# Performance work log

Hardware: AMD Instinct MI355X
Metric: run time of the kernel (lower is better)

## Reference

```python
import jax, jax.numpy as jnp
import numpy as np

N = 100000
E = 1600000
D_IN = 64
D_HID = 64
D_OUT = 64


def setup_inputs() -> dict:
    key = jax.random.key(0)
    ks = jax.random.split(key, 12)
    x = jax.random.normal(ks[0], (N, D_IN), dtype=jnp.float32)
    edge_index = jax.random.randint(ks[1], (2, E), 0, N, dtype=jnp.int64)
    s1 = 1.0 / np.sqrt(D_IN)
    s2 = 1.0 / np.sqrt(D_HID)
    return {
        "x": x,
        "edge_index": edge_index,
        "W1l": jax.random.uniform(ks[2], (D_HID, D_IN), jnp.float32, -s1, s1),
        "b1l": jax.random.uniform(ks[3], (D_HID,), jnp.float32, -s1, s1),
        "W1r": jax.random.uniform(ks[4], (D_HID, D_IN), jnp.float32, -s1, s1),
        "W2l": jax.random.uniform(ks[5], (D_HID, D_HID), jnp.float32, -s2, s2),
        "b2l": jax.random.uniform(ks[6], (D_HID,), jnp.float32, -s2, s2),
        "W2r": jax.random.uniform(ks[7], (D_HID, D_HID), jnp.float32, -s2, s2),
        "Wout": jax.random.uniform(ks[8], (D_OUT, D_HID), jnp.float32, -s2, s2),
        "bout": jax.random.uniform(ks[9], (D_OUT,), jnp.float32, -s2, s2),
        "drop": 0,
    }


def _sage_conv(x, src, dst, Wl, bl, Wr, n_nodes):
    # PyG SAGEConv, aggr='mean': out = lin_l(mean_j x_j) + lin_r(x_i)
    msg = x[src]                                            # [E, d] gather
    agg = jax.ops.segment_sum(msg, dst, num_segments=n_nodes)
    deg = jax.ops.segment_sum(jnp.ones((src.shape[0],), x.dtype), dst,
                              num_segments=n_nodes)
    mean = agg / jnp.maximum(deg, 1.0)[:, None]             # empty neighborhoods -> 0
    return mean @ Wl.T + bl + x @ Wr.T


def reference(x, edge_index, W1l, b1l, W1r, W2l, b2l, W2r, Wout, bout, drop):
    src, dst = edge_index[0], edge_index[1]
    n = x.shape[0]
    # dropout is identity in eval mode (training=False); drop unused
    h = jax.nn.relu(_sage_conv(x, src, dst, W1l, b1l, W1r, n))
    h = jax.nn.relu(_sage_conv(h, src, dst, W2l, b2l, W2r, n))
    logits = h @ Wout.T + bout
    return jax.nn.log_softmax(logits, axis=1)
```

## Files before the change

kernel.cpp:

```cpp
#include <hip/hip_runtime.h>


#define TB 256
#define TBA 1024
#define NBINA 256
#define XFB 512
#define CAPC 32
#define NBPAD 1024
#define SP 68

typedef __attribute__((ext_vector_type(8))) short bf16x8;
typedef __attribute__((ext_vector_type(4))) float f32x4;
typedef __attribute__((ext_vector_type(2))) float f32x2;

__device__ __forceinline__ unsigned short bf16c(float f) {
  union { float f; unsigned u; } v; v.f = f;
  unsigned r = (v.u + 0x7FFFu + ((v.u >> 16) & 1u)) >> 16;
  return (unsigned short)r;
}

__device__ __forceinline__ bf16x8 ld_bf8(const float* p) {
  float4 a = *(const float4*)p;
  float4 b = *(const float4*)(p + 4);
  bf16x8 r;
  r[0] = bf16c(a.x); r[1] = bf16c(a.y); r[2] = bf16c(a.z); r[3] = bf16c(a.w);
  r[4] = bf16c(b.x); r[5] = bf16c(b.y); r[6] = bf16c(b.z); r[7] = bf16c(b.w);
  return r;
}

__device__ __forceinline__ float bflo(unsigned u) { return __uint_as_float(u << 16); }
__device__ __forceinline__ float bfhi(unsigned u) { return __uint_as_float(u & 0xFFFF0000u); }
__device__ __forceinline__ unsigned bfpk(float lo, float hi) {
  return (unsigned)bf16c(lo) | ((unsigned)bf16c(hi) << 16);
}

__global__ __launch_bounds__(1024) void k_binA(
    const int* __restrict__ ei, int E,
    int* __restrict__ cellcnt, unsigned int* __restrict__ bucketData, int NB) {
  __shared__ int lcnt[NBPAD];
  __shared__ int s_nz;
  if (threadIdx.x == 0) s_nz = 0;
  for (int i = threadIdx.x; i < NBPAD; i += TBA) lcnt[i] = 0;
  __syncthreads();
  int nz = 0;
  for (int i = threadIdx.x; i < 2048; i += TBA) nz |= ei[2 * i + 1];
  if (nz) atomicOr(&s_nz, 1);
  __syncthreads();
  bool m64 = (s_nz == 0);
  int bb = blockIdx.x;

  long long e0 = (long long)E * bb / NBINA;
  long long e1 = (long long)E * (bb + 1) / NBINA;
  for (long long e = e0 + threadIdx.x; e < e1; e += TBA) {
    int src, dst;
    if (m64) {
      src = ((const int2*)ei)[e].x;
      dst = ((const int2*)ei)[(long long)E + e].x;
    } else {
      src = ei[e];
      dst = ei[(long long)E + e];
    }
    int b = dst >> 7;
    int pos = atomicAdd(&lcnt[b], 1);
    if (pos < CAPC)
      bucketData[((size_t)b * NBINA + bb) * CAPC + pos] =
          ((unsigned)(dst & 127) << 24) | (unsigned)src;
  }
  __syncthreads();
  for (int b = threadIdx.x; b < NB; b += TBA) cellcnt[bb * NBPAD + b] = lcnt[b];
}

__global__ __launch_bounds__(256) void k_binB(
    const unsigned int* __restrict__ bucketData, const int* __restrict__ cellcnt,
    int* __restrict__ colp, int* __restrict__ cnt) {
  __shared__ unsigned int slice[128 * SP];
  __shared__ int lcnt[128];
  int b = blockIdx.x;
  for (int i = threadIdx.x; i < 128; i += TB) lcnt[i] = 0;
  __syncthreads();
  int c = cellcnt[threadIdx.x * NBPAD + b];
  if (c > CAPC) c = CAPC;
  const uint4* cell4 =
      (const uint4*)(bucketData + ((size_t)b * NBINA + threadIdx.x) * CAPC);
#pragma unroll
  for (int k4 = 0; k4 < CAPC / 4; ++k4) {
    if (k4 * 4 >= c) break;
    uint4 r4 = cell4[k4];
#pragma unroll
    for (int j = 0; j < 4; ++j) {
      int k = k4 * 4 + j;
      if (k < c) {
        unsigned rec = (&r4.x)[j];
        int dl = rec >> 24;
        int pos = atomicAdd(&lcnt[dl], 1);
        if (pos < 64) slice[dl * SP + pos] = rec & 0xFFFFFFu;
      }
    }
  }
  __syncthreads();
  size_t obase = (size_t)b * (128 * 64);
  for (int i = threadIdx.x * 4; i < 128 * 64; i += TB * 4) {
    int node = i >> 6, j = i & 63;
    *(uint4*)(colp + obase + i) = *(const uint4*)(slice + node * SP + j);
  }
  int node0 = b << 7;
  for (int i = threadIdx.x; i < 128; i += TB) cnt[node0 + i] = lcnt[i];
}

__global__ __launch_bounds__(256) void k_xform_f32(
    const float* __restrict__ xin, const float* __restrict__ Wl,
    const float* __restrict__ Wr, const float* __restrict__ bl,
    unsigned short* __restrict__ y, unsigned short* __restrict__ zout, int n) {
  int lane = threadIdx.x & 63;
  int quad = lane >> 4, m = lane & 15;
  int w0 = (blockIdx.x * blockDim.x + threadIdx.x) >> 6;
  int nw = (gridDim.x * blockDim.x) >> 6;

  bf16x8 bfrag[8][2];
  float bias[4];
#pragma unroll
  for (int t = 0; t < 8; ++t) {
    const float* W = (t < 4) ? Wl : Wr;
    int row = (t & 3) * 16 + m;
#pragma unroll
    for (int s = 0; s < 2; ++s)
      bfrag[t][s] = ld_bf8(W + row * 64 + s * 32 + quad * 8);
  }
#pragma unroll
  for (int t = 0; t < 4; ++t) bias[t] = bl[t * 16 + m];

  int nT = (n + 15) >> 4;
  for (int tile = w0; tile < nT; tile += nw) {
    int node0 = tile << 4;
    int mrow = node0 + m;
    if (mrow >= n) mrow = n - 1;
    const float* xr = xin + (size_t)mrow * 64;
    bf16x8 a0 = ld_bf8(xr + quad * 8);
    bf16x8 a1 = ld_bf8(xr + 32 + quad * 8);

    f32x4 acc[8];
#pragma unroll
    for (int t = 0; t < 8; ++t) {
      f32x4 z4 = {0.f, 0.f, 0.f, 0.f};
      z4 = __builtin_amdgcn_mfma_f32_16x16x32_bf16(a0, bfrag[t][0], z4, 0, 0, 0);
      acc[t] = __builtin_amdgcn_mfma_f32_16x16x32_bf16(a1, bfrag[t][1], z4, 0, 0, 0);
    }

#pragma unroll
    for (int r = 0; r < 4; ++r) {
      int node = node0 + quad * 4 + r;
      if (node >= n) break;
      size_t rb = (size_t)node * 64 + m;
#pragma unroll
      for (int t = 0; t < 4; ++t) y[rb + t * 16] = bf16c(acc[t][r]);
#pragma unroll
      for (int t = 0; t < 4; ++t) zout[rb + t * 16] = bf16c(acc[t + 4][r] + bias[t]);
    }
  }
}

__global__ __launch_bounds__(256) void k_xform_b16(
    const unsigned short* zin, const float* __restrict__ Wl,
    const float* __restrict__ Wr, const float* __restrict__ bl,
    unsigned short* __restrict__ y, unsigned short* zout, int n) {
  int lane = threadIdx.x & 63;
  int quad = lane >> 4, m = lane & 15;
  int w0 = (blockIdx.x * blockDim.x + threadIdx.x) >> 6;
  int nw = (gridDim.x * blockDim.x) >> 6;

  bf16x8 bfrag[8][2];
  float bias[4];
#pragma unroll
  for (int t = 0; t < 8; ++t) {
    const float* W = (t < 4) ? Wl : Wr;
    int row = (t & 3) * 16 + m;
#pragma unroll
    for (int s = 0; s < 2; ++s)
      bfrag[t][s] = ld_bf8(W + row * 64 + s * 32 + quad * 8);
  }
#pragma unroll
  for (int t = 0; t < 4; ++t) bias[t] = bl[t * 16 + m];

  int nT = (n + 15) >> 4;
  for (int tile = w0; tile < nT; tile += nw) {
    int node0 = tile << 4;
    int mrow = node0 + m;
    if (mrow >= n) mrow = n - 1;
    const unsigned short* xr = zin + (size_t)mrow * 64;
    bf16x8 a0 = *(const bf16x8*)(xr + quad * 8);
    bf16x8 a1 = *(const bf16x8*)(xr + 32 + quad * 8);

    f32x4 acc[8];
#pragma unroll
    for (int t = 0; t < 8; ++t) {
      f32x4 z4 = {0.f, 0.f, 0.f, 0.f};
      z4 = __builtin_amdgcn_mfma_f32_16x16x32_bf16(a0, bfrag[t][0], z4, 0, 0, 0);
      acc[t] = __builtin_amdgcn_mfma_f32_16x16x32_bf16(a1, bfrag[t][1], z4, 0, 0, 0);
    }

#pragma unroll
    for (int r = 0; r < 4; ++r) {
      int node = node0 + quad * 4 + r;
      if (node >= n) break;
      size_t rb = (size_t)node * 64 + m;
#pragma unroll
      for (int t = 0; t < 4; ++t) y[rb + t * 16] = bf16c(acc[t][r]);
#pragma unroll
      for (int t = 0; t < 4; ++t) zout[rb + t * 16] = bf16c(acc[t + 4][r] + bias[t]);
    }
  }
}

__global__ __launch_bounds__(256) void k_aggr(
    const unsigned short* __restrict__ yb, const int* __restrict__ cnt,
    const int* __restrict__ colp, unsigned short* zio, int n) {
  const unsigned int* y = (const unsigned int*)yb;
  int lane = threadIdx.x & 63;
  int wv = (blockIdx.x * blockDim.x + threadIdx.x) >> 6;
  int g16 = lane & 48;
  int lig = lane & 15;
  int sub = lig >> 3;
  int fo = (lig & 7) * 4;

  int node = (wv << 2) + (g16 >> 4);
  bool act = node < n;
  int cn = act ? node : 0;
  int deg = cnt[cn];
  int jcap = deg < 64 ? deg : 64;
  size_t crow = (size_t)cn << 6;
  int cidxA = colp[crow + lig];
  int cidxB = colp[crow + 16 + lig];

  int wmax = jcap;
  wmax = max(wmax, __shfl_xor(wmax, 16, 64));
  wmax = max(wmax, __shfl_xor(wmax, 32, 64));

  f32x2 acc[4];
#pragma unroll
  for (int k = 0; k < 4; ++k) acc[k] = (f32x2){0.f, 0.f};

#define ACCUM(U)                                             \
  do {                                                       \
    acc[0] += (f32x2){bflo((U).x), bfhi((U).x)};             \
    acc[1] += (f32x2){bflo((U).y), bfhi((U).y)};             \
    acc[2] += (f32x2){bflo((U).z), bfhi((U).z)};             \
    acc[3] += (f32x2){bflo((U).w), bfhi((U).w)};             \
  } while (0)

#pragma unroll
  for (int s = 0; s < 32; s += 2) {
    int slot = s + sub;
    int c = (s < 16) ? __shfl(cidxA, g16 | slot, 64)
                     : __shfl(cidxB, g16 | (slot - 16), 64);
    if (slot < jcap) {
      uint4 v = *(const uint4*)(y + ((size_t)c << 5) + fo);
      ACCUM(v);
    }
  }
  if (wmax > 32) {
    int cidxC = colp[crow + 32 + lig];
    int cidxD = colp[crow + 48 + lig];
    {
      int lim = (wmax < 48 ? wmax : 48) - 32;
      for (int s = 0; s < lim; s += 2) {
        int slot = s + sub;
        int c = __shfl(cidxC, g16 | slot, 64);
        if (slot + 32 < jcap) {
          uint4 v = *(const uint4*)(y + ((size_t)c << 5) + fo);
          ACCUM(v);
        }
      }
    }
    if (wmax > 48) {
      int lim = wmax - 48;
      for (int s = 0; s < lim; s += 2) {
        int slot = s + sub;
        int c = __shfl(cidxD, g16 | slot, 64);
        if (slot + 48 < jcap) {
          uint4 v = *(const uint4*)(y + ((size_t)c << 5) + fo);
          ACCUM(v);
        }
      }
    }
  }
#undef ACCUM

#pragma unroll
  for (int k = 0; k < 4; ++k) {
    acc[k].x += __shfl_xor(acc[k].x, 8, 64);
    acc[k].y += __shfl_xor(acc[k].y, 8, 64);
  }

  if (act && sub == 0) {
    float inv = (deg > 0) ? 1.0f / (float)deg : 0.f;
    unsigned int* zp = (unsigned int*)(zio + ((size_t)node << 6)) + fo;
    uint4 zv = *(uint4*)zp;
    zv.x = bfpk(fmaxf(fmaf(acc[0].x, inv, bflo(zv.x)), 0.f),
                fmaxf(fmaf(acc[0].y, inv, bfhi(zv.x)), 0.f));
    zv.y = bfpk(fmaxf(fmaf(acc[1].x, inv, bflo(zv.y)), 0.f),
                fmaxf(fmaf(acc[1].y, inv, bfhi(zv.y)), 0.f));
    zv.z = bfpk(fmaxf(fmaf(acc[2].x, inv, bflo(zv.z)), 0.f),
                fmaxf(fmaf(acc[2].y, inv, bfhi(zv.z)), 0.f));
    zv.w = bfpk(fmaxf(fmaf(acc[3].x, inv, bflo(zv.w)), 0.f),
                fmaxf(fmaf(acc[3].y, inv, bfhi(zv.w)), 0.f));
    *(uint4*)zp = zv;
  }
}

__global__ __launch_bounds__(256) void k_out(
    const unsigned short* __restrict__ h, const float* __restrict__ Wo,
    const float* __restrict__ bo, float* __restrict__ out, int n) {
  int lane = threadIdx.x & 63;
  int quad = lane >> 4, m = lane & 15;
  int w0 = (blockIdx.x * blockDim.x + threadIdx.x) >> 6;
  int nw = (gridDim.x * blockDim.x) >> 6;

  bf16x8 bfrag[4][2];
  float bias[4];
#pragma unroll
  for (int t = 0; t < 4; ++t) {
    int row = t * 16 + m;
#pragma unroll
    for (int s = 0; s < 2; ++s)
      bfrag[t][s] = ld_bf8(Wo + row * 64 + s * 32 + quad * 8);
    bias[t] = bo[t * 16 + m];
  }

  int nT = (n + 15) >> 4;
  for (int tile = w0; tile < nT; tile += nw) {
    int node0 = tile << 4;
    int mrow = node0 + m;
    if (mrow >= n) mrow = n - 1;
    const unsigned short* xr = h + (size_t)mrow * 64;
    bf16x8 a0 = *(const bf16x8*)(xr + quad * 8);
    bf16x8 a1 = *(const bf16x8*)(xr + 32 + quad * 8);

    f32x4 acc[4];
#pragma unroll
    for (int t = 0; t < 4; ++t) {
      f32x4 z4 = {0.f, 0.f, 0.f, 0.f};
      z4 = __builtin_amdgcn_mfma_f32_16x16x32_bf16(a0, bfrag[t][0], z4, 0, 0, 0);
      acc[t] = __builtin_amdgcn_mfma_f32_16x16x32_bf16(a1, bfrag[t][1], z4, 0, 0, 0);
    }

#pragma unroll
    for (int r = 0; r < 4; ++r) {
      int node = node0 + quad * 4 + r;
      if (node >= n) break;
      float l0 = acc[0][r] + bias[0];
      float l1 = acc[1][r] + bias[1];
      float l2 = acc[2][r] + bias[2];
      float l3 = acc[3][r] + bias[3];
      float mx = fmaxf(fmaxf(l0, l1), fmaxf(l2, l3));
#pragma unroll
      for (int off = 1; off <= 8; off <<= 1) mx = fmaxf(mx, __shfl_xor(mx, off, 64));
      float s = expf(l0 - mx) + expf(l1 - mx) + expf(l2 - mx) + expf(l3 - mx);
#pragma unroll
      for (int off = 1; off <= 8; off <<= 1) s += __shfl_xor(s, off, 64);
      float ls = logf(s);
      size_t rb = (size_t)node * 64 + m;
      out[rb + 0]  = l0 - mx - ls;
      out[rb + 16] = l1 - mx - ls;
      out[rb + 32] = l2 - mx - ls;
      out[rb + 48] = l3 - mx - ls;
    }
  }
}

extern "C" void kernel_launch(void* const* d_in, const int* in_sizes, int n_in,
                              void* d_out, int out_size, void* d_ws, size_t ws_size,
                              hipStream_t stream) {
  const float* x    = (const float*)d_in[0];
  const int*   ei   = (const int*)d_in[1];
  const float* W1l  = (const float*)d_in[2];
  const float* b1l  = (const float*)d_in[3];
  const float* W1r  = (const float*)d_in[4];
  const float* W2l  = (const float*)d_in[5];
  const float* b2l  = (const float*)d_in[6];
  const float* W2r  = (const float*)d_in[7];
  const float* Wout = (const float*)d_in[8];
  const float* bout = (const float*)d_in[9];
  int N = in_sizes[0] / 64;
  int E = in_sizes[1] / 2;
  int NB = (N + 127) >> 7;

  char* p = (char*)d_ws;
  auto carve = [&](size_t bytes) {
    char* r = p;
    p += (bytes + 255) & ~(size_t)255;
    return r;
  };
  int* cellcnt       = (int*)carve((size_t)NBINA * NBPAD * 4);
  int* cnt           = (int*)carve((size_t)NB * 128 * 4);
  int* colp          = (int*)carve((size_t)NB * 128 * 64 * 4);
  unsigned short* y  = (unsigned short*)carve((size_t)N * 64 * 2);
  unsigned short* z  = (unsigned short*)carve((size_t)N * 64 * 2);
  unsigned int* bucketData = (unsigned int*)carve((size_t)NB * NBINA * CAPC * 4);

  int aggr_blocks = (N + 15) / 16;
  k_binA<<<NBINA, TBA, 0, stream>>>(ei, E, cellcnt, bucketData, NB);
  k_binB<<<NB, TB, 0, stream>>>(bucketData, cellcnt, colp, cnt);
  k_xform_f32<<<XFB, TB, 0, stream>>>(x, W1l, W1r, b1l, y, z, N);
  k_aggr<<<aggr_blocks, TB, 0, stream>>>(y, cnt, colp, z, N);
  k_xform_b16<<<XFB, TB, 0, stream>>>(z, W2l, W2r, b2l, y, z, N);
  k_aggr<<<aggr_blocks, TB, 0, stream>>>(y, cnt, colp, z, N);
  k_out<<<XFB, TB, 0, stream>>>(z, Wout, bout, (float*)d_out, N);
}
```

Before: 236.9 us.

## Fuse bucket finalization into aggregation kernel, drop materialized CSR arrays

Merges the second binning pass (k_binB) into the aggregation kernel. Each layer's aggregation block now rebuilds its 128-node neighbor slice in shared memory from the bucket data and gathers neighbor features straight from that slice. This removes one launch and the write and read of the padded colp and cnt arrays. In exchange the slice construction is done twice (once per layer), blocks become coarser (128 nodes each, one per wave group over 8 iterations), and neighbor indices come from LDS instead of register shuffles.

Result: slower. 266.8 us (+12.6%).

```diff
diff --git a/kernel.cpp b/kernel.cpp
--- a/kernel.cpp
+++ b/kernel.cpp
@@ -70,9 +70,113 @@
   for (int b = threadIdx.x; b < NB; b += TBA) cellcnt[bb * NBPAD + b] = lcnt[b];
 }
 
-__global__ __launch_bounds__(256) void k_binB(
+__global__ __launch_bounds__(256) void k_xform_f32(
+    const float* __restrict__ xin, const float* __restrict__ Wl,
+    const float* __restrict__ Wr, const float* __restrict__ bl,
+    unsigned short* __restrict__ y, unsigned short* __restrict__ zout, int n) {
+  int lane = threadIdx.x & 63;
+  int quad = lane >> 4, m = lane & 15;
+  int w0 = (blockIdx.x * blockDim.x + threadIdx.x) >> 6;
+  int nw = (gridDim.x * blockDim.x) >> 6;
+
+  bf16x8 bfrag[8][2];
+  float bias[4];
+#pragma unroll
+  for (int t = 0; t < 8; ++t) {
+    const float* W = (t < 4) ? Wl : Wr;
+    int row = (t & 3) * 16 + m;
+#pragma unroll
+    for (int s = 0; s < 2; ++s)
+      bfrag[t][s] = ld_bf8(W + row * 64 + s * 32 + quad * 8);
+  }
+#pragma unroll
+  for (int t = 0; t < 4; ++t) bias[t] = bl[t * 16 + m];
+
+  int nT = (n + 15) >> 4;
+  for (int tile = w0; tile < nT; tile += nw) {
+    int node0 = tile << 4;
+    int mrow = node0 + m;
+    if (mrow >= n) mrow = n - 1;
+    const float* xr = xin + (size_t)mrow * 64;
+    bf16x8 a0 = ld_bf8(xr + quad * 8);
+    bf16x8 a1 = ld_bf8(xr + 32 + quad * 8);
+
+    f32x4 acc[8];
+#pragma unroll
+    for (int t = 0; t < 8; ++t) {
+      f32x4 z4 = {0.f, 0.f, 0.f, 0.f};
+      z4 = __builtin_amdgcn_mfma_f32_16x16x32_bf16(a0, bfrag[t][0], z4, 0, 0, 0);
+      acc[t] = __builtin_amdgcn_mfma_f32_16x16x32_bf16(a1, bfrag[t][1], z4, 0, 0, 0);
+    }
+
+#pragma unroll
+    for (int r = 0; r < 4; ++r) {
+      int node = node0 + quad * 4 + r;
+      if (node >= n) break;
+      size_t rb = (size_t)node * 64 + m;
+#pragma unroll
+      for (int t = 0; t < 4; ++t) y[rb + t * 16] = bf16c(acc[t][r]);
+#pragma unroll
+      for (int t = 0; t < 4; ++t) zout[rb + t * 16] = bf16c(acc[t + 4][r] + bias[t]);
+    }
+  }
+}
+
+__global__ __launch_bounds__(256) void k_xform_b16(
+    const unsigned short* zin, const float* __restrict__ Wl,
+    const float* __restrict__ Wr, const float* __restrict__ bl,
+    unsigned short* __restrict__ y, unsigned short* zout, int n) {
+  int lane = threadIdx.x & 63;
+  int quad = lane >> 4, m = lane & 15;
+  int w0 = (blockIdx.x * blockDim.x + threadIdx.x) >> 6;
+  int nw = (gridDim.x * blockDim.x) >> 6;
+
+  bf16x8 bfrag[8][2];
+  float bias[4];
+#pragma unroll
+  for (int t = 0; t < 8; ++t) {
+    const float* W = (t < 4) ? Wl : Wr;
+    int row = (t & 3) * 16 + m;
+#pragma unroll
+    for (int s = 0; s < 2; ++s)
+      bfrag[t][s] = ld_bf8(W + row * 64 + s * 32 + quad * 8);
+  }
+#pragma unroll
+  for (int t = 0; t < 4; ++t) bias[t] = bl[t * 16 + m];
+
+  int nT = (n + 15) >> 4;
+  for (int tile = w0; tile < nT; tile += nw) {
+    int node0 = tile << 4;
+    int mrow = node0 + m;
+    if (mrow >= n) mrow = n - 1;
+    const unsigned short* xr = zin + (size_t)mrow * 64;
+    bf16x8 a0 = *(const bf16x8*)(xr + quad * 8);
+    bf16x8 a1 = *(const bf16x8*)(xr + 32 + quad * 8);
+
+    f32x4 acc[8];
+#pragma unroll
+    for (int t = 0; t < 8; ++t) {
+      f32x4 z4 = {0.f, 0.f, 0.f, 0.f};
+      z4 = __builtin_amdgcn_mfma_f32_16x16x32_bf16(a0, bfrag[t][0], z4, 0, 0, 0);
+      acc[t] = __builtin_amdgcn_mfma_f32_16x16x32_bf16(a1, bfrag[t][1], z4, 0, 0, 0);
+    }
+
+#pragma unroll
+    for (int r = 0; r < 4; ++r) {
+      int node = node0 + quad * 4 + r;
+      if (node >= n) break;
+      size_t rb = (size_t)node * 64 + m;
+#pragma unroll
+      for (int t = 0; t < 4; ++t) y[rb + t * 16] = bf16c(acc[t][r]);
+#pragma unroll
+      for (int t = 0; t < 4; ++t) zout[rb + t * 16] = bf16c(acc[t + 4][r] + bias[t]);
+    }
+  }
+}
+
+__global__ __launch_bounds__(256, 4) void k_bag(
     const unsigned int* __restrict__ bucketData, const int* __restrict__ cellcnt,
-    int* __restrict__ colp, int* __restrict__ cnt) {
+    const unsigned short* __restrict__ yb, unsigned short* zio, int n) {
   __shared__ unsigned int slice[128 * SP];
   __shared__ int lcnt[128];
   int b = blockIdx.x;
@@ -98,146 +202,29 @@
     }
   }
   __syncthreads();
-  size_t obase = (size_t)b * (128 * 64);
-  for (int i = threadIdx.x * 4; i < 128 * 64; i += TB * 4) {
-    int node = i >> 6, j = i & 63;
-    *(uint4*)(colp + obase + i) = *(const uint4*)(slice + node * SP + j);
-  }
-  int node0 = b << 7;
-  for (int i = threadIdx.x; i < 128; i += TB) cnt[node0 + i] = lcnt[i];
-}
-
-__global__ __launch_bounds__(256) void k_xform_f32(
-    const float* __restrict__ xin, const float* __restrict__ Wl,
-    const float* __restrict__ Wr, const float* __restrict__ bl,
-    unsigned short* __restrict__ y, unsigned short* __restrict__ zout, int n) {
-  int lane = threadIdx.x & 63;
-  int quad = lane >> 4, m = lane & 15;
-  int w0 = (blockIdx.x * blockDim.x + threadIdx.x) >> 6;
-  int nw = (gridDim.x * blockDim.x) >> 6;
-
-  bf16x8 bfrag[8][2];
-  float bias[4];
-#pragma unroll
-  for (int t = 0; t < 8; ++t) {
-    const float* W = (t < 4) ? Wl : Wr;
-    int row = (t & 3) * 16 + m;
-#pragma unroll
-    for (int s = 0; s < 2; ++s)
-      bfrag[t][s] = ld_bf8(W + row * 64 + s * 32 + quad * 8);
-  }
-#pragma unroll
-  for (int t = 0; t < 4; ++t) bias[t] = bl[t * 16 + m];
-
-  int nT = (n + 15) >> 4;
-  for (int tile = w0; tile < nT; tile += nw) {
-    int node0 = tile << 4;
-    int mrow = node0 + m;
-    if (mrow >= n) mrow = n - 1;
-    const float* xr = xin + (size_t)mrow * 64;
-    bf16x8 a0 = ld_bf8(xr + quad * 8);
-    bf16x8 a1 = ld_bf8(xr + 32 + quad * 8);
-
-    f32x4 acc[8];
-#pragma unroll
-    for (int t = 0; t < 8; ++t) {
-      f32x4 z4 = {0.f, 0.f, 0.f, 0.f};
-      z4 = __builtin_amdgcn_mfma_f32_16x16x32_bf16(a0, bfrag[t][0], z4, 0, 0, 0);
-      acc[t] = __builtin_amdgcn_mfma_f32_16x16x32_bf16(a1, bfrag[t][1], z4, 0, 0, 0);
-    }
-
-#pragma unroll
-    for (int r = 0; r < 4; ++r) {
-      int node = node0 + quad * 4 + r;
-      if (node >= n) break;
-      size_t rb = (size_t)node * 64 + m;
-#pragma unroll
-      for (int t = 0; t < 4; ++t) y[rb + t * 16] = bf16c(acc[t][r]);
-#pragma unroll
-      for (int t = 0; t < 4; ++t) zout[rb + t * 16] = bf16c(acc[t + 4][r] + bias[t]);
-    }
-  }
-}
-
-__global__ __launch_bounds__(256) void k_xform_b16(
-    const unsigned short* zin, const float* __restrict__ Wl,
-    const float* __restrict__ Wr, const float* __restrict__ bl,
-    unsigned short* __restrict__ y, unsigned short* zout, int n) {
-  int lane = threadIdx.x & 63;
-  int quad = lane >> 4, m = lane & 15;
-  int w0 = (blockIdx.x * blockDim.x + threadIdx.x) >> 6;
-  int nw = (gridDim.x * blockDim.x) >> 6;
-
-  bf16x8 bfrag[8][2];
-  float bias[4];
-#pragma unroll
-  for (int t = 0; t < 8; ++t) {
-    const float* W = (t < 4) ? Wl : Wr;
-    int row = (t & 3) * 16 + m;
-#pragma unroll
-    for (int s = 0; s < 2; ++s)
-      bfrag[t][s] = ld_bf8(W + row * 64 + s * 32 + quad * 8);
-  }
-#pragma unroll
-  for (int t = 0; t < 4; ++t) bias[t] = bl[t * 16 + m];
-
-  int nT = (n + 15) >> 4;
-  for (int tile = w0; tile < nT; tile += nw) {
-    int node0 = tile << 4;
-    int mrow = node0 + m;
-    if (mrow >= n) mrow = n - 1;
-    const unsigned short* xr = zin + (size_t)mrow * 64;
-    bf16x8 a0 = *(const bf16x8*)(xr + quad * 8);
-    bf16x8 a1 = *(const bf16x8*)(xr + 32 + quad * 8);
-
-    f32x4 acc[8];
-#pragma unroll
-    for (int t = 0; t < 8; ++t) {
-      f32x4 z4 = {0.f, 0.f, 0.f, 0.f};
-      z4 = __builtin_amdgcn_mfma_f32_16x16x32_bf16(a0, bfrag[t][0], z4, 0, 0, 0);
-      acc[t] = __builtin_amdgcn_mfma_f32_16x16x32_bf16(a1, bfrag[t][1], z4, 0, 0, 0);
-    }
-
-#pragma unroll
-    for (int r = 0; r < 4; ++r) {
-      int node = node0 + quad * 4 + r;
-      if (node >= n) break;
-      size_t rb = (size_t)node * 64 + m;
-#pragma unroll
-      for (int t = 0; t < 4; ++t) y[rb + t * 16] = bf16c(acc[t][r]);
-#pragma unroll
-      for (int t = 0; t < 4; ++t) zout[rb + t * 16] = bf16c(acc[t + 4][r] + bias[t]);
-    }
-  }
-}
-
-__global__ __launch_bounds__(256) void k_aggr(
-    const unsigned short* __restrict__ yb, const int* __restrict__ cnt,
-    const int* __restrict__ colp, unsigned short* zio, int n) {
+
   const unsigned int* y = (const unsigned int*)yb;
   int lane = threadIdx.x & 63;
-  int wv = (blockIdx.x * blockDim.x + threadIdx.x) >> 6;
+  int w = threadIdx.x >> 6;
   int g16 = lane & 48;
   int lig = lane & 15;
   int sub = lig >> 3;
   int fo = (lig & 7) * 4;
 
-  int node = (wv << 2) + (g16 >> 4);
-  bool act = node < n;
-  int cn = act ? node : 0;
-  int deg = cnt[cn];
-  int jcap = deg < 64 ? deg : 64;
-  size_t crow = (size_t)cn << 6;
-  int cidxA = colp[crow + lig];
-  int cidxB = colp[crow + 16 + lig];
-
-  int wmax = jcap;
-  wmax = max(wmax, __shfl_xor(wmax, 16, 64));
-  wmax = max(wmax, __shfl_xor(wmax, 32, 64));
-
-  f32x2 acc[4];
-#pragma unroll
-  for (int k = 0; k < 4; ++k) acc[k] = (f32x2){0.f, 0.f};
+  for (int j = 0; j < 8; ++j) {
+    int nb = (w << 5) + (j << 2) + (g16 >> 4);
+    int node = (b << 7) + nb;
+    bool act = node < n;
+    int deg = lcnt[nb];
+    int jcap = deg < 64 ? deg : 64;
+
+    int wmax = jcap;
+    wmax = max(wmax, __shfl_xor(wmax, 16, 64));
+    wmax = max(wmax, __shfl_xor(wmax, 32, 64));
+
+    f32x2 acc[4];
+#pragma unroll
+    for (int k = 0; k < 4; ++k) acc[k] = (f32x2){0.f, 0.f};
 
 #define ACCUM(U)                                             \
   do {                                                       \
@@ -248,62 +235,46 @@
   } while (0)
 
 #pragma unroll
-  for (int s = 0; s < 32; s += 2) {
-    int slot = s + sub;
-    int c = (s < 16) ? __shfl(cidxA, g16 | slot, 64)
-                     : __shfl(cidxB, g16 | (slot - 16), 64);
-    if (slot < jcap) {
-      uint4 v = *(const uint4*)(y + ((size_t)c << 5) + fo);
-      ACCUM(v);
-    }
-  }
-  if (wmax > 32) {
-    int cidxC = colp[crow + 32 + lig];
-    int cidxD = colp[crow + 48 + lig];
-    {
-      int lim = (wmax < 48 ? wmax : 48) - 32;
-      for (int s = 0; s < lim; s += 2) {
+    for (int s = 0; s < 32; s += 2) {
+      int slot = s + sub;
+      int cidx = (int)slice[nb * SP + slot];
+      if (slot < jcap) {
+        uint4 v = *(const uint4*)(y + ((size_t)cidx << 5) + fo);
+        ACCUM(v);
+      }
+    }
+    if (wmax > 32) {
+      for (int s = 32; s < wmax; s += 2) {
         int slot = s + sub;
-        int c = __shfl(cidxC, g16 | slot, 64);
-        if (slot + 32 < jcap) {
-          uint4 v = *(const uint4*)(y + ((size_t)c << 5) + fo);
+        int cidx = (int)slice[nb * SP + slot];
+        if (slot < jcap) {
+          uint4 v = *(const uint4*)(y + ((size_t)cidx << 5) + fo);
           ACCUM(v);
         }
       }
     }
-    if (wmax > 48) {
-      int lim = wmax - 48;
-      for (int s = 0; s < lim; s += 2) {
-        int slot = s + sub;
-        int c = __shfl(cidxD, g16 | slot, 64);
-        if (slot + 48 < jcap) {
-          uint4 v = *(const uint4*)(y + ((size_t)c << 5) + fo);
-          ACCUM(v);
-        }
-      }
-    }
-  }
 #undef ACCUM
 
 #pragma unroll
-  for (int k = 0; k < 4; ++k) {
-    acc[k].x += __shfl_xor(acc[k].x, 8, 64);
-    acc[k].y += __shfl_xor(acc[k].y, 8, 64);
-  }
-
-  if (act && sub == 0) {
-    float inv = (deg > 0) ? 1.0f / (float)deg : 0.f;
-    unsigned int* zp = (unsigned int*)(zio + ((size_t)node << 6)) + fo;
-    uint4 zv = *(uint4*)zp;
-    zv.x = bfpk(fmaxf(fmaf(acc[0].x, inv, bflo(zv.x)), 0.f),
-                fmaxf(fmaf(acc[0].y, inv, bfhi(zv.x)), 0.f));
-    zv.y = bfpk(fmaxf(fmaf(acc[1].x, inv, bflo(zv.y)), 0.f),
-                fmaxf(fmaf(acc[1].y, inv, bfhi(zv.y)), 0.f));
-    zv.z = bfpk(fmaxf(fmaf(acc[2].x, inv, bflo(zv.z)), 0.f),
-                fmaxf(fmaf(acc[2].y, inv, bfhi(zv.z)), 0.f));
-    zv.w = bfpk(fmaxf(fmaf(acc[3].x, inv, bflo(zv.w)), 0.f),
-                fmaxf(fmaf(acc[3].y, inv, bfhi(zv.w)), 0.f));
-    *(uint4*)zp = zv;
+    for (int k = 0; k < 4; ++k) {
+      acc[k].x += __shfl_xor(acc[k].x, 8, 64);
+      acc[k].y += __shfl_xor(acc[k].y, 8, 64);
+    }
+
+    if (act && sub == 0) {
+      float inv = (deg > 0) ? 1.0f / (float)deg : 0.f;
+      unsigned int* zp = (unsigned int*)(zio + ((size_t)node << 6)) + fo;
+      uint4 zv = *(uint4*)zp;
+      zv.x = bfpk(fmaxf(fmaf(acc[0].x, inv, bflo(zv.x)), 0.f),
+                  fmaxf(fmaf(acc[0].y, inv, bfhi(zv.x)), 0.f));
+      zv.y = bfpk(fmaxf(fmaf(acc[1].x, inv, bflo(zv.y)), 0.f),
+                  fmaxf(fmaf(acc[1].y, inv, bfhi(zv.y)), 0.f));
+      zv.z = bfpk(fmaxf(fmaf(acc[2].x, inv, bflo(zv.z)), 0.f),
+                  fmaxf(fmaf(acc[2].y, inv, bfhi(zv.z)), 0.f));
+      zv.w = bfpk(fmaxf(fmaf(acc[3].x, inv, bflo(zv.w)), 0.f),
+                  fmaxf(fmaf(acc[3].y, inv, bfhi(zv.w)), 0.f));
+      *(uint4*)zp = zv;
+    }
   }
 }
 
@@ -391,18 +362,14 @@
     return r;
   };
   int* cellcnt       = (int*)carve((size_t)NBINA * NBPAD * 4);
-  int* cnt           = (int*)carve((size_t)NB * 128 * 4);
-  int* colp          = (int*)carve((size_t)NB * 128 * 64 * 4);
   unsigned short* y  = (unsigned short*)carve((size_t)N * 64 * 2);
   unsigned short* z  = (unsigned short*)carve((size_t)N * 64 * 2);
   unsigned int* bucketData = (unsigned int*)carve((size_t)NB * NBINA * CAPC * 4);
 
-  int aggr_blocks = (N + 15) / 16;
   k_binA<<<NBINA, TBA, 0, stream>>>(ei, E, cellcnt, bucketData, NB);
-  k_binB<<<NB, TB, 0, stream>>>(bucketData, cellcnt, colp, cnt);
   k_xform_f32<<<XFB, TB, 0, stream>>>(x, W1l, W1r, b1l, y, z, N);
-  k_aggr<<<aggr_blocks, TB, 0, stream>>>(y, cnt, colp, z, N);
+  k_bag<<<NB, TB, 0, stream>>>(bucketData, cellcnt, y, z, N);
   k_xform_b16<<<XFB, TB, 0, stream>>>(z, W2l, W2r, b2l, y, z, N);
-  k_aggr<<<aggr_blocks, TB, 0, stream>>>(y, cnt, colp, z, N);
+  k_bag<<<NB, TB, 0, stream>>>(bucketData, cellcnt, y, z, N);
   k_out<<<XFB, TB, 0, stream>>>(z, Wout, bout, (float*)d_out, N);
 }
```
